# Kernel tuning notes

Hardware: AMD Instinct MI355X
Metric: run time of the kernel (lower is better)

Reference implementation:

```python
import jax, jax.numpy as jnp
import numpy as np

N, G = 10000, 200          # nodes, graphs
EL, EG = 160000, 500000    # local / global edges
S, V = 256, 64             # scalar / vector hidden dims
NA, NB = 16, 5             # atom types, bond types


def _lin(k, i, o):
    return (jax.random.normal(k, (i, o), jnp.float32) / np.sqrt(i))


def scatter_mean(vals, idx, num_segments):
    # vals: [N, ...]; idx: [N] int
    sums = jax.ops.segment_sum(vals, idx, num_segments=num_segments)
    cnt = jax.ops.segment_sum(jnp.ones((vals.shape[0],), vals.dtype), idx,
                              num_segments=num_segments)
    cnt = jnp.maximum(cnt, 1.0).reshape((-1,) + (1,) * (vals.ndim - 1))
    return sums / cnt


def calc_edge_attrs(edge_index, pos):
    src, tgt = edge_index[0], edge_index[1]
    r = pos[tgt] - pos[src]                      # [E,3]
    a = (pos[tgt] * pos[src]).sum(-1)            # [E]
    d = jnp.sqrt(jnp.clip((r ** 2).sum(-1), 1e-6))
    r_norm = r / d[:, None]
    return d, a, r_norm


def setup_inputs() -> dict:
    key = jax.random.key(0)
    ks = jax.random.split(key, 24)
    inp = {}
    inp["x"] = jax.random.normal(ks[0], (N, NA), jnp.float32)
    inp["t"] = jax.random.uniform(ks[1], (G, 1), jnp.float32)
    inp["pos"] = jax.random.normal(ks[2], (N, 3), jnp.float32)
    eil = jax.random.randint(ks[3], (2, EL), 0, N)
    eig = jax.random.randint(ks[4], (2, EG), 0, N)
    # avoid self-edges so edge distances are strictly positive (safe sqrt grads)
    eig = eig.at[1].set(jnp.where(eig[1] == eig[0], (eig[1] + 1) % N, eig[1]))
    eil = eil.at[1].set(jnp.where(eil[1] == eil[0], (eil[1] + 1) % N, eil[1]))
    inp["edge_index_local"] = eil
    inp["edge_index_global"] = eig
    inp["edge_attr_global"] = jax.random.normal(ks[5], (EG, NB), jnp.float32)
    inp["batch"] = jnp.sort(jax.random.randint(ks[6], (N,), 0, G))
    # learned parameters
    inp["W_time"], inp["b_time"] = _lin(ks[7], 1, S), jnp.zeros((S,), jnp.float32)
    inp["W_atom"], inp["b_atom"] = _lin(ks[8], NA, S), jnp.zeros((S,), jnp.float32)
    inp["W_at"], inp["b_at"] = _lin(ks[9], S, S), jnp.zeros((S,), jnp.float32)
    inp["W_shared"], inp["b_shared"] = _lin(ks[10], S, S), jnp.zeros((S,), jnp.float32)
    inp["W_b0"], inp["b_b0"] = _lin(ks[11], S + 1, S), jnp.zeros((S,), jnp.float32)
    inp["W_b1"], inp["b_b1"] = _lin(ks[12], S, 2 * NB), jnp.zeros((2 * NB,), jnp.float32)
    inp["W_coord"] = _lin(ks[13], V, 2)           # no bias
    inp["W_atoms"], inp["b_atoms"] = _lin(ks[14], S, 2 * NA), jnp.zeros((2 * NA,), jnp.float32)
    return inp


def reference(x, t, pos, edge_attr_global, W_time, b_time, W_atom, b_atom,
              W_at, b_at, W_shared, b_shared, W_b0, b_b0, W_b1, b_b1,
              W_coord, W_atoms, b_atoms,
              edge_index_local, edge_index_global, batch):
    # --- trunk: center positions, embed atoms + time ---
    pos = pos - scatter_mean(pos, batch, G)[batch]
    temb = t @ W_time + b_time                    # [G,S]
    tnode = temb[batch]                           # [N,S]
    s = x @ W_atom + b_atom
    s = (s + tnode) @ W_at + b_at                 # [N,S]
    # --- edge attrs (gather-compute pattern feeding the GNN) ---
    d_l, a_l, rn_l = calc_edge_attrs(edge_index_local, pos)
    d_g, a_g, rn_g = calc_edge_attrs(edge_index_global, pos)
    # GNN stand-in (identity on s, v, p): v initialized to zeros as in original
    v = jnp.zeros((N, 3, V), s.dtype)
    # --- prediction head ---
    s = jax.nn.silu(s @ W_shared + b_shared)
    j, i = edge_index_global[0], edge_index_global[1]
    d = jnp.sqrt(((pos[i] - pos[j]) ** 2).sum(-1, keepdims=True))  # [EG,1]
    edge = jnp.concatenate([s[i] + s[j], d], axis=-1)              # [EG,S+1]
    bonds = jax.nn.silu(edge @ W_b0 + b_b0) @ W_b1 + b_b1          # [EG,2*NB]
    bonds_pred, bonds_eps = bonds[:, :NB], bonds[:, NB:]
    coords = jnp.einsum('nkv,vo->nko', v, W_coord)                 # [N,3,2]
    coords = coords - scatter_mean(coords, batch, G)[batch]
    coords_eps0, coords_eps1 = coords[..., 0], coords[..., 1]      # [N,3]
    atoms = s @ W_atoms + b_atoms                                  # [N,2*NA]
    atoms_eps, atoms_pred = atoms[:, :NA], atoms[:, NA:]
    pos_c = pos - scatter_mean(pos, batch, G)[batch]
    coords_pred = pos_c + coords_eps1
    return (coords_pred, coords_eps0, atoms_pred, atoms_eps,
            bonds_pred, bonds_eps, d_l, rn_l, a_g, rn_g)
```

## Files before the change

### kernel.cpp

```cpp
#include <hip/hip_runtime.h>
#include <hip/hip_bf16.h>

typedef __hip_bfloat16 bf16;
typedef short bf16x8 __attribute__((ext_vector_type(8)));
typedef float f32x4 __attribute__((ext_vector_type(4)));
typedef _Float16 f16x2 __attribute__((ext_vector_type(2)));
typedef _Float16 f16x8 __attribute__((ext_vector_type(8)));

#define N_NODES  10000
#define G_GRAPHS 200
#define EL_EDGES 160000
#define EG_EDGES 500000
#define S_DIM    256
#define APAD     264

#define BONDS2        7813
#define LOCAL_BLOCKS  625

#define WS_FLAG   0
#define WS_POSC   1024
#define WS_WDH    31232
#define WS_W1F    31488
#define WS_BB0R   33536
#define WS_BB1    34304
#define WS_WATOM  34560
#define WS_WTIME  38656
#define WS_BTIME  38912
#define WS_BATOM  39168
#define WS_BAT    39424
#define WS_BSH    39680
#define WS_BATOMS 39936
#define WS_T      40000
#define WS_X      40448
#define WT_AT     200448
#define WT_SH     233216
#define WT_B0     265984
#define WT_ATOMS  298752
#define WS_H      303968
#define WS_END_FLOATS 1583968

#define O_CPRED 0
#define O_CEPS  30000
#define O_APRED 60000
#define O_AEPS  220000
#define O_BPRED 380000
#define O_BEPS  2880000
#define O_DL    5380000
#define O_RNL   5540000
#define O_AG    6020000
#define O_RNG   6520000

__device__ __forceinline__ float b2f(bf16 v) { return __bfloat162float(v); }
__device__ __forceinline__ bf16  f2b(float v) { return __float2bfloat16(v); }
__device__ __forceinline__ unsigned short bbits(float v) {
    bf16 b = f2b(v);
    return *reinterpret_cast<unsigned short*>(&b);
}
__device__ __forceinline__ unsigned short h16bits(float v) {
    _Float16 h = (_Float16)v;
    return *reinterpret_cast<unsigned short*>(&h);
}
__device__ __forceinline__ float ldin(const void* p, int idx, int isf32) {
    return isf32 ? ((const float*)p)[idx] : b2f(((const bf16*)p)[idx]);
}
__device__ __forceinline__ void stout(void* out, int f32o, size_t idx, float v) {
    if (f32o) ((float*)out)[idx] = v;
    else      ((bf16*)out)[idx]  = f2b(v);
}
__device__ __forceinline__ float silu(float p) {
    return p * __builtin_amdgcn_rcpf(1.0f + __expf(-p));
}
__device__ __forceinline__ _Float16 h_exp2(_Float16 x) {
    _Float16 r;
    asm("v_exp_f16 %0, %1" : "=v"(r) : "v"(x));
    return r;
}
__device__ __forceinline__ _Float16 h_rcp(_Float16 x) {
    _Float16 r;
    asm("v_rcp_f16 %0, %1" : "=v"(r) : "v"(x));
    return r;
}
__device__ __forceinline__ _Float16 h_silu(_Float16 p) {
    const _Float16 nlog2e = (_Float16)(-1.44269504f);
    _Float16 ex = h_exp2(p * nlog2e);
    return p * h_rcp((_Float16)1.0f + ex);
}
__device__ __forceinline__ int dtype_f32(const void* tt) {
    const unsigned short* q = (const unsigned short*)tt;
    int c = 0;
#pragma unroll
    for (int z = 0; z < 32; ++z) c += (q[z] >= 0x4000) ? 1 : 0;
    return c > 0;
}

__global__ void k_prep(const void* __restrict__ x, const void* __restrict__ tt,
                       const void* __restrict__ W_time, const void* __restrict__ b_time,
                       const void* __restrict__ W_atom, const void* __restrict__ b_atom,
                       const void* __restrict__ W_at, const void* __restrict__ b_at,
                       const void* __restrict__ W_shared, const void* __restrict__ b_shared,
                       const void* __restrict__ W_b0, const void* __restrict__ b_b0,
                       const void* __restrict__ W_b1, const void* __restrict__ b_b1,
                       const void* __restrict__ W_atoms, const void* __restrict__ b_atoms,
                       float* __restrict__ ws) {
    const int t = blockIdx.x * blockDim.x + threadIdx.x;
    const int f = dtype_f32(tt);
    if (t == 0) ws[WS_FLAG] = f ? 1.0f : 0.0f;
    if (t < 65536) {
        const int k = t >> 8, n = t & 255;
        ((unsigned short*)(ws + WT_AT))[n * 256 + k] = bbits(ldin(W_at, t, f));
        ((unsigned short*)(ws + WT_SH))[n * 256 + k] = bbits(ldin(W_shared, t, f));
        ((unsigned short*)(ws + WT_B0))[n * 256 + k] = bbits(ldin(W_b0, t, f));
    }
    if (t < 160000) ws[WS_X + t] = ldin(x, t, f);
    if (t < 8192) {
        const int k = t >> 5, n = t & 31;
        ((unsigned short*)(ws + WT_ATOMS))[n * 256 + k] = bbits(ldin(W_atoms, t, f));
    }
    if (t < 4096) {
        const int i = t & 7, l16 = (t >> 3) & 15, quad = (t >> 7) & 3, ts = t >> 9;
        const int k = ts * 32 + quad * 8 + i;
        float v = (l16 < 10) ? ldin(W_b1, k * 10 + l16, f) : 0.0f;
        ((unsigned short*)(ws + WS_W1F))[t] = h16bits(v);
    }
    if (t < 4096) ws[WS_WATOM + t] = ldin(W_atom, t, f);
    if (t < 256) {
        ((unsigned short*)(ws + WS_WDH))[t] = h16bits(ldin(W_b0, 65536 + t, f));
        ws[WS_BB0R + t] = ldin(b_b0, t, f);
        ws[WS_WTIME + t] = ldin(W_time, t, f);
        ws[WS_BTIME + t] = ldin(b_time, t, f);
        ws[WS_BATOM + t] = ldin(b_atom, t, f);
        ws[WS_BAT + t]   = ldin(b_at, t, f);
        ws[WS_BSH + t]   = ldin(b_shared, t, f);
    }
    if (t < 200) ws[WS_T + t] = ldin(tt, t, f);
    if (t < 32)  ws[WS_BATOMS + t] = ldin(b_atoms, t, f);
    if (t < 16)  ws[WS_BB1 + t] = (t < 10) ? ldin(b_b1, t, f) : 0.0f;
}

__global__ void k_pos(const void* __restrict__ pos, const int* __restrict__ batch,
                      float* __restrict__ ws, void* __restrict__ out) {
    const int g = blockIdx.x;
    const int f32o = ws[WS_FLAG] != 0.0f;
    __shared__ int s_lo, s_hi;
    __shared__ float wsum[4][3];
    __shared__ float mean[3];
    if (threadIdx.x == 0) {
        int lo = 0, hi = N_NODES;
        while (lo < hi) { int m = (lo + hi) >> 1; if (batch[m] < g) lo = m + 1; else hi = m; }
        s_lo = lo;
        int lo2 = lo; hi = N_NODES;
        while (lo2 < hi) { int m = (lo2 + hi) >> 1; if (batch[m] < g + 1) lo2 = m + 1; else hi = m; }
        s_hi = lo2;
    }
    __syncthreads();
    const int lo = s_lo, hi = s_hi, cnt = hi - lo;
    float sx = 0.f, sy = 0.f, sz = 0.f;
    for (int n = lo + threadIdx.x; n < hi; n += 256) {
        sx += ldin(pos, n * 3 + 0, f32o);
        sy += ldin(pos, n * 3 + 1, f32o);
        sz += ldin(pos, n * 3 + 2, f32o);
    }
#pragma unroll
    for (int off = 32; off > 0; off >>= 1) {
        sx += __shfl_down(sx, off);
        sy += __shfl_down(sy, off);
        sz += __shfl_down(sz, off);
    }
    if ((threadIdx.x & 63) == 0) {
        wsum[threadIdx.x >> 6][0] = sx;
        wsum[threadIdx.x >> 6][1] = sy;
        wsum[threadIdx.x >> 6][2] = sz;
    }
    __syncthreads();
    if (threadIdx.x == 0) {
        float inv = 1.0f / (float)max(cnt, 1);
        mean[0] = (wsum[0][0] + wsum[1][0] + wsum[2][0] + wsum[3][0]) * inv;
        mean[1] = (wsum[0][1] + wsum[1][1] + wsum[2][1] + wsum[3][1]) * inv;
        mean[2] = (wsum[0][2] + wsum[1][2] + wsum[2][2] + wsum[3][2]) * inv;
    }
    __syncthreads();
    for (int n = lo + threadIdx.x; n < hi; n += 256) {
#pragma unroll
        for (int k = 0; k < 3; ++k) {
            float p = ldin(pos, n * 3 + k, f32o) - mean[k];
            ws[WS_POSC + n * 3 + k] = p;
            stout(out, f32o, O_CPRED + n * 3 + k, p);
            stout(out, f32o, O_CEPS + n * 3 + k, 0.0f);
        }
    }
}

__global__ __launch_bounds__(256) void k_node(
    const int* __restrict__ batch, const float* __restrict__ ws,
    unsigned short* __restrict__ h_out, void* __restrict__ out) {
    __shared__ unsigned short actA[16][APAD];
    __shared__ unsigned short actB[16][APAD];
    const int tid = threadIdx.x;
    const int wave = tid >> 6, lane = tid & 63;
    const int quad = lane >> 4, l16 = lane & 15;
    const int row0 = blockIdx.x * 16;

    {
        const int r = tid >> 4;
        const int c0 = (tid & 15) * 16;
        const int g = row0 + r;
        float tb = ws[WS_T + batch[g]];
        float xr[16];
#pragma unroll
        for (int k = 0; k < 16; ++k) xr[k] = ws[WS_X + g * 16 + k];
        for (int cc = 0; cc < 16; cc += 4) {
            const int c = c0 + cc;
            float a0 = ws[WS_BATOM + c + 0] + tb * ws[WS_WTIME + c + 0] + ws[WS_BTIME + c + 0];
            float a1 = ws[WS_BATOM + c + 1] + tb * ws[WS_WTIME + c + 1] + ws[WS_BTIME + c + 1];
            float a2 = ws[WS_BATOM + c + 2] + tb * ws[WS_WTIME + c + 2] + ws[WS_BTIME + c + 2];
            float a3 = ws[WS_BATOM + c + 3] + tb * ws[WS_WTIME + c + 3] + ws[WS_BTIME + c + 3];
#pragma unroll
            for (int k = 0; k < 16; ++k) {
                float4 w4 = *(const float4*)(ws + WS_WATOM + k * S_DIM + c);
                a0 += xr[k] * w4.x; a1 += xr[k] * w4.y;
                a2 += xr[k] * w4.z; a3 += xr[k] * w4.w;
            }
            actA[r][c + 0] = bbits(a0); actA[r][c + 1] = bbits(a1);
            actA[r][c + 2] = bbits(a2); actA[r][c + 3] = bbits(a3);
        }
    }
    __syncthreads();

    const unsigned short* wt_at = (const unsigned short*)(ws + WT_AT);
    const unsigned short* wt_sh = (const unsigned short*)(ws + WT_SH);
    const unsigned short* wt_b0 = (const unsigned short*)(ws + WT_B0);
    const unsigned short* wt_am = (const unsigned short*)(ws + WT_ATOMS);
    const int n0 = wave * 64;

    {
        f32x4 acc[4] = {};
        for (int kk = 0; kk < S_DIM; kk += 32) {
            const int k = kk + quad * 8;
            bf16x8 a = *(const bf16x8*)&actA[l16][k];
#pragma unroll
            for (int nt = 0; nt < 4; ++nt) {
                bf16x8 b = *(const bf16x8*)(wt_at + (size_t)(n0 + nt * 16 + l16) * S_DIM + k);
                acc[nt] = __builtin_amdgcn_mfma_f32_16x16x32_bf16(a, b, acc[nt], 0, 0, 0);
            }
        }
#pragma unroll
        for (int nt = 0; nt < 4; ++nt) {
            const int n = n0 + nt * 16 + l16;
            const float bv = ws[WS_BAT + n];
#pragma unroll
            for (int r = 0; r < 4; ++r)
                actB[quad * 4 + r][n] = bbits(acc[nt][r] + bv);
        }
    }
    __syncthreads();

    {
        f32x4 acc[4] = {};
        for (int kk = 0; kk < S_DIM; kk += 32) {
            const int k = kk + quad * 8;
            bf16x8 a = *(const bf16x8*)&actB[l16][k];
#pragma unroll
            for (int nt = 0; nt < 4; ++nt) {
                bf16x8 b = *(const bf16x8*)(wt_sh + (size_t)(n0 + nt * 16 + l16) * S_DIM + k);
                acc[nt] = __builtin_amdgcn_mfma_f32_16x16x32_bf16(a, b, acc[nt], 0, 0, 0);
            }
        }
        __syncthreads();
#pragma unroll
        for (int nt = 0; nt < 4; ++nt) {
            const int n = n0 + nt * 16 + l16;
            const float bv = ws[WS_BSH + n];
#pragma unroll
            for (int r = 0; r < 4; ++r)
                actA[quad * 4 + r][n] = bbits(silu(acc[nt][r] + bv));
        }
    }
    __syncthreads();

    {
        f32x4 acc[4] = {};
        for (int kk = 0; kk < S_DIM; kk += 32) {
            const int k = kk + quad * 8;
            bf16x8 a = *(const bf16x8*)&actA[l16][k];
#pragma unroll
            for (int nt = 0; nt < 4; ++nt) {
                bf16x8 b = *(const bf16x8*)(wt_b0 + (size_t)(n0 + nt * 16 + l16) * S_DIM + k);
                acc[nt] = __builtin_amdgcn_mfma_f32_16x16x32_bf16(a, b, acc[nt], 0, 0, 0);
            }
        }
        _Float16* hp = (_Float16*)h_out;
#pragma unroll
        for (int nt = 0; nt < 4; ++nt) {
            const int n = n0 + nt * 16 + l16;
            const float bh = 0.5f * ws[WS_BB0R + n];
#pragma unroll
            for (int r = 0; r < 4; ++r) {
                const int g = row0 + quad * 4 + r;
                hp[(size_t)g * 256 + n] = (_Float16)(acc[nt][r] + bh);
            }
        }
    }

    if (wave < 2) {
        f32x4 acc = {};
        const int n = wave * 16 + l16;
        for (int kk = 0; kk < S_DIM; kk += 32) {
            const int k = kk + quad * 8;
            bf16x8 a = *(const bf16x8*)&actA[l16][k];
            bf16x8 b = *(const bf16x8*)(wt_am + (size_t)n * S_DIM + k);
            acc = __builtin_amdgcn_mfma_f32_16x16x32_bf16(a, b, acc, 0, 0, 0);
        }
        const float bv = ws[WS_BATOMS + n];
        const int f32o = ws[WS_FLAG] != 0.0f;
#pragma unroll
        for (int r = 0; r < 4; ++r) {
            const int g = row0 + quad * 4 + r;
            float v = acc[r] + bv;
            if (n < 16) stout(out, f32o, O_AEPS + (size_t)g * 16 + n, v);
            else        stout(out, f32o, O_APRED + (size_t)g * 16 + (n - 16), v);
        }
    }
}

union H8 { f16x8 v; f16x2 p[4]; };

__global__ __launch_bounds__(256, 4) void k_edges(const int* __restrict__ eig,
                                                  const int* __restrict__ eil,
                                                  const float* __restrict__ ws,
                                                  const _Float16* __restrict__ h,
                                                  void* __restrict__ out) {
    const int f32o = ws[WS_FLAG] != 0.0f;

    if (blockIdx.x >= BONDS2) {
        const int e = (blockIdx.x - BONDS2) * 256 + threadIdx.x;
        const float* posc = ws + WS_POSC;
        const int s = eil[e];
        const int t = eil[EL_EDGES + e];
        float rx = posc[t * 3 + 0] - posc[s * 3 + 0];
        float ry = posc[t * 3 + 1] - posc[s * 3 + 1];
        float rz = posc[t * 3 + 2] - posc[s * 3 + 2];
        float dsq = rx * rx + ry * ry + rz * rz;
        float d = sqrtf(fmaxf(dsq, 1e-6f));
        float inv = 1.0f / d;
        stout(out, f32o, O_DL + e, d);
        stout(out, f32o, O_RNL + (size_t)e * 3 + 0, rx * inv);
        stout(out, f32o, O_RNL + (size_t)e * 3 + 1, ry * inv);
        stout(out, f32o, O_RNL + (size_t)e * 3 + 2, rz * inv);
        return;
    }

    const int wave = threadIdx.x >> 6, lane = threadIdx.x & 63;
    const int quad = lane >> 4, l16 = lane & 15;
    const int e0 = blockIdx.x * 64 + wave * 16;
    if (e0 >= EG_EDGES) return;

    const int e = e0 + l16;
    const int j = eig[e];
    const int i = eig[EG_EDGES + e];

    const float* posc = ws + WS_POSC;
    float pix = posc[i * 3 + 0], piy = posc[i * 3 + 1], piz = posc[i * 3 + 2];
    float pjx = posc[j * 3 + 0], pjy = posc[j * 3 + 1], pjz = posc[j * 3 + 2];
    float rx = pix - pjx, ry = piy - pjy, rz = piz - pjz;
    float dsq = rx * rx + ry * ry + rz * rz;
    float dbf = sqrtf(dsq);
    if (quad == 0) {
        float ag = pix * pjx + piy * pjy + piz * pjz;
        float inv = 1.0f / sqrtf(fmaxf(dsq, 1e-6f));
        stout(out, f32o, O_AG + e, ag);
        stout(out, f32o, O_RNG + (size_t)e * 3 + 0, rx * inv);
        stout(out, f32o, O_RNG + (size_t)e * 3 + 1, ry * inv);
        stout(out, f32o, O_RNG + (size_t)e * 3 + 2, rz * inv);
    }

    const _Float16 hd = (_Float16)dbf;
    const f16x2 d2 = {hd, hd};

    const _Float16* hi_row = h + (size_t)i * 256 + quad * 8;
    const _Float16* hj_row = h + (size_t)j * 256 + quad * 8;
    const _Float16* wdh = (const _Float16*)(ws + WS_WDH) + quad * 8;
    const _Float16* w1f = (const _Float16*)(ws + WS_W1F) + (quad * 16 + l16) * 8;

    f32x4 acc = {};
#pragma unroll 2
    for (int t = 0; t < 8; ++t) {
        H8 A, B, W;
        A.v = *(const f16x8*)(hi_row + t * 32);
        B.v = *(const f16x8*)(hj_row + t * 32);
        W.v = *(const f16x8*)(wdh + t * 32);
        f16x8 WB = *(const f16x8*)(w1f + t * 512);
        f16x2 p2[4];
#pragma unroll
        for (int pp = 0; pp < 4; ++pp)
            p2[pp] = (A.p[pp] + B.p[pp]) + d2 * W.p[pp];
        f16x8 U = {h_silu(p2[0][0]), h_silu(p2[0][1]),
                   h_silu(p2[1][0]), h_silu(p2[1][1]),
                   h_silu(p2[2][0]), h_silu(p2[2][1]),
                   h_silu(p2[3][0]), h_silu(p2[3][1])};
        acc = __builtin_amdgcn_mfma_f32_16x16x32_f16(U, WB, acc, 0, 0, 0);
    }

    if (l16 < 10) {
        const float bv = ws[WS_BB1 + l16];
#pragma unroll
        for (int r = 0; r < 4; ++r) {
            const int er = e0 + quad * 4 + r;
            float v = acc[r] + bv;
            if (l16 < 5) stout(out, f32o, O_BPRED + (size_t)er * 5 + l16, v);
            else         stout(out, f32o, O_BEPS + (size_t)er * 5 + (l16 - 5), v);
        }
    }
}

extern "C" void kernel_launch(void* const* d_in, const int* in_sizes, int n_in,
                              void* d_out, int out_size, void* d_ws, size_t ws_size,
                              hipStream_t stream) {
    const void* x        = d_in[0];
    const void* t        = d_in[1];
    const void* pos      = d_in[2];
    const int*  eil      = (const int*)d_in[3];
    const int*  eig      = (const int*)d_in[4];
    const int*  batch    = (const int*)d_in[6];
    const void* W_time   = d_in[7];
    const void* b_time   = d_in[8];
    const void* W_atom   = d_in[9];
    const void* b_atom   = d_in[10];
    const void* W_at     = d_in[11];
    const void* b_at     = d_in[12];
    const void* W_shared = d_in[13];
    const void* b_shared = d_in[14];
    const void* W_b0     = d_in[15];
    const void* b_b0     = d_in[16];
    const void* W_b1     = d_in[17];
    const void* b_b1     = d_in[18];
    const void* W_atoms  = d_in[20];
    const void* b_atoms  = d_in[21];
    (void)in_sizes; (void)n_in; (void)out_size;

    const size_t NEED = (size_t)WS_END_FLOATS * sizeof(float);
    if (ws_size < NEED) return;

    float* ws = (float*)d_ws;
    unsigned short* hbuf = (unsigned short*)(ws + WS_H);

    k_prep<<<640, 256, 0, stream>>>(x, t, W_time, b_time, W_atom, b_atom,
                                    W_at, b_at, W_shared, b_shared, W_b0, b_b0,
                                    W_b1, b_b1, W_atoms, b_atoms, ws);
    k_pos<<<G_GRAPHS, 256, 0, stream>>>(pos, batch, ws, d_out);
    k_node<<<N_NODES / 16, 256, 0, stream>>>(batch, ws, hbuf, d_out);
    k_edges<<<BONDS2 + LOCAL_BLOCKS, 256, 0, stream>>>(
        eig, eil, ws, (const _Float16*)hbuf, d_out);
}
```

Baseline: 252.6 us.

## Store per-node bond projection in FP8 and gather it in edge kernel

The per-node bond-layer projection h is now written as packed FP8 (4 bytes per 4 channels) instead of fp16, with a permuted channel layout (CHAN) so each lane's 8 consecutive bytes map onto the MFMA K-slice. The edge kernel gathers 8 bytes per row instead of 16 and unpacks them to f32. It then does the add, distance term and SiLU in f32 before packing to f16 for the MFMA. This halves gather traffic on the dominant 500k-edge random reads and shrinks the workspace. The cost is FP8 quantization error in the hidden activations and extra conversion and f32 ALU work per edge.

```diff
diff --git a/kernel.cpp b/kernel.cpp
--- a/kernel.cpp
+++ b/kernel.cpp
@@ -4,8 +4,10 @@
 typedef __hip_bfloat16 bf16;
 typedef short bf16x8 __attribute__((ext_vector_type(8)));
 typedef float f32x4 __attribute__((ext_vector_type(4)));
+typedef float f32x2 __attribute__((ext_vector_type(2)));
 typedef _Float16 f16x2 __attribute__((ext_vector_type(2)));
 typedef _Float16 f16x8 __attribute__((ext_vector_type(8)));
+typedef __fp16 fp16x2 __attribute__((ext_vector_type(2)));
 
 #define N_NODES  10000
 #define G_GRAPHS 200
@@ -19,7 +21,7 @@
 
 #define WS_FLAG   0
 #define WS_POSC   1024
-#define WS_WDH    31232
+#define WS_WD     31232
 #define WS_W1F    31488
 #define WS_BB0R   33536
 #define WS_BB1    34304
@@ -37,7 +39,9 @@
 #define WT_B0     265984
 #define WT_ATOMS  298752
 #define WS_H      303968
-#define WS_END_FLOATS 1583968
+#define WS_END_FLOATS 944224
+
+#define CHAN(S)    ((((S) >> 6) << 6) + (((S) & 3) << 4) + (((S) & 63) >> 2))
 
 #define O_CPRED 0
 #define O_CEPS  30000
@@ -70,20 +74,11 @@
 __device__ __forceinline__ float silu(float p) {
     return p * __builtin_amdgcn_rcpf(1.0f + __expf(-p));
 }
-__device__ __forceinline__ _Float16 h_exp2(_Float16 x) {
-    _Float16 r;
-    asm("v_exp_f16 %0, %1" : "=v"(r) : "v"(x));
-    return r;
-}
-__device__ __forceinline__ _Float16 h_rcp(_Float16 x) {
-    _Float16 r;
-    asm("v_rcp_f16 %0, %1" : "=v"(r) : "v"(x));
-    return r;
-}
-__device__ __forceinline__ _Float16 h_silu(_Float16 p) {
-    const _Float16 nlog2e = (_Float16)(-1.44269504f);
-    _Float16 ex = h_exp2(p * nlog2e);
-    return p * h_rcp((_Float16)1.0f + ex);
+__device__ __forceinline__ f32x2 silu2(f32x2 p) {
+    f32x2 u;
+    u[0] = p[0] * __builtin_amdgcn_rcpf(1.0f + __expf(-p[0]));
+    u[1] = p[1] * __builtin_amdgcn_rcpf(1.0f + __expf(-p[1]));
+    return u;
 }
 __device__ __forceinline__ int dtype_f32(const void* tt) {
     const unsigned short* q = (const unsigned short*)tt;
@@ -117,14 +112,14 @@
         ((unsigned short*)(ws + WT_ATOMS))[n * 256 + k] = bbits(ldin(W_atoms, t, f));
     }
     if (t < 4096) {
-        const int i = t & 7, l16 = (t >> 3) & 15, quad = (t >> 7) & 3, ts = t >> 9;
-        const int k = ts * 32 + quad * 8 + i;
-        float v = (l16 < 10) ? ldin(W_b1, k * 10 + l16, f) : 0.0f;
+        const int i = t & 7, lc = (t >> 3) & 15, q = (t >> 7) & 3, ts = t >> 9;
+        const int s = ts * 32 + q * 8 + i;
+        float v = (lc < 10) ? ldin(W_b1, CHAN(s) * 10 + lc, f) : 0.0f;
         ((unsigned short*)(ws + WS_W1F))[t] = h16bits(v);
     }
     if (t < 4096) ws[WS_WATOM + t] = ldin(W_atom, t, f);
     if (t < 256) {
-        ((unsigned short*)(ws + WS_WDH))[t] = h16bits(ldin(W_b0, 65536 + t, f));
+        ws[WS_WD + t]   = ldin(W_b0, 65536 + CHAN(t), f);
         ws[WS_BB0R + t] = ldin(b_b0, t, f);
         ws[WS_WTIME + t] = ldin(W_time, t, f);
         ws[WS_BTIME + t] = ldin(b_time, t, f);
@@ -192,7 +187,7 @@
 
 __global__ __launch_bounds__(256) void k_node(
     const int* __restrict__ batch, const float* __restrict__ ws,
-    unsigned short* __restrict__ h_out, void* __restrict__ out) {
+    unsigned int* __restrict__ h_out, void* __restrict__ out) {
     __shared__ unsigned short actA[16][APAD];
     __shared__ unsigned short actB[16][APAD];
     const int tid = threadIdx.x;
@@ -288,16 +283,16 @@
                 acc[nt] = __builtin_amdgcn_mfma_f32_16x16x32_bf16(a, b, acc[nt], 0, 0, 0);
             }
         }
-        _Float16* hp = (_Float16*)h_out;
-#pragma unroll
-        for (int nt = 0; nt < 4; ++nt) {
-            const int n = n0 + nt * 16 + l16;
-            const float bh = 0.5f * ws[WS_BB0R + n];
-#pragma unroll
-            for (int r = 0; r < 4; ++r) {
-                const int g = row0 + quad * 4 + r;
-                hp[(size_t)g * 256 + n] = (_Float16)(acc[nt][r] + bh);
-            }
+        float bh[4];
+#pragma unroll
+        for (int nt = 0; nt < 4; ++nt) bh[nt] = 0.5f * ws[WS_BB0R + n0 + nt * 16 + l16];
+#pragma unroll
+        for (int r = 0; r < 4; ++r) {
+            const int g = row0 + quad * 4 + r;
+            int w = 0;
+            w = __builtin_amdgcn_cvt_pk_fp8_f32(acc[0][r] + bh[0], acc[1][r] + bh[1], w, false);
+            w = __builtin_amdgcn_cvt_pk_fp8_f32(acc[2][r] + bh[2], acc[3][r] + bh[3], w, true);
+            h_out[(size_t)g * 64 + wave * 16 + l16] = (unsigned int)w;
         }
     }
 
@@ -322,12 +317,12 @@
     }
 }
 
-union H8 { f16x8 v; f16x2 p[4]; };
+union U8 { f16x8 v; fp16x2 p[4]; };
 
 __global__ __launch_bounds__(256, 4) void k_edges(const int* __restrict__ eig,
                                                   const int* __restrict__ eil,
                                                   const float* __restrict__ ws,
-                                                  const _Float16* __restrict__ h,
+                                                  const unsigned char* __restrict__ h,
                                                   void* __restrict__ out) {
     const int f32o = ws[WS_FLAG] != 0.0f;
 
@@ -363,7 +358,7 @@
     float pjx = posc[j * 3 + 0], pjy = posc[j * 3 + 1], pjz = posc[j * 3 + 2];
     float rx = pix - pjx, ry = piy - pjy, rz = piz - pjz;
     float dsq = rx * rx + ry * ry + rz * rz;
-    float dbf = sqrtf(dsq);
+    float dgeo = sqrtf(dsq);
     if (quad == 0) {
         float ag = pix * pjx + piy * pjy + piz * pjz;
         float inv = 1.0f / sqrtf(fmaxf(dsq, 1e-6f));
@@ -373,31 +368,42 @@
         stout(out, f32o, O_RNG + (size_t)e * 3 + 2, rz * inv);
     }
 
-    const _Float16 hd = (_Float16)dbf;
-    const f16x2 d2 = {hd, hd};
-
-    const _Float16* hi_row = h + (size_t)i * 256 + quad * 8;
-    const _Float16* hj_row = h + (size_t)j * 256 + quad * 8;
-    const _Float16* wdh = (const _Float16*)(ws + WS_WDH) + quad * 8;
+    const f32x2 d2 = {dgeo, dgeo};
+    const unsigned char* hi_row = h + (size_t)i * 256;
+    const unsigned char* hj_row = h + (size_t)j * 256;
     const _Float16* w1f = (const _Float16*)(ws + WS_W1F) + (quad * 16 + l16) * 8;
 
     f32x4 acc = {};
 #pragma unroll 2
     for (int t = 0; t < 8; ++t) {
-        H8 A, B, W;
-        A.v = *(const f16x8*)(hi_row + t * 32);
-        B.v = *(const f16x8*)(hj_row + t * 32);
-        W.v = *(const f16x8*)(wdh + t * 32);
-        f16x8 WB = *(const f16x8*)(w1f + t * 512);
-        f16x2 p2[4];
-#pragma unroll
-        for (int pp = 0; pp < 4; ++pp)
-            p2[pp] = (A.p[pp] + B.p[pp]) + d2 * W.p[pp];
-        f16x8 U = {h_silu(p2[0][0]), h_silu(p2[0][1]),
-                   h_silu(p2[1][0]), h_silu(p2[1][1]),
-                   h_silu(p2[2][0]), h_silu(p2[2][1]),
-                   h_silu(p2[3][0]), h_silu(p2[3][1])};
-        acc = __builtin_amdgcn_mfma_f32_16x16x32_f16(U, WB, acc, 0, 0, 0);
+        const int k = quad * 8 + t * 32;
+        uint2 ua = *(const uint2*)(hi_row + k);
+        uint2 ub = *(const uint2*)(hj_row + k);
+        float4 wA = *(const float4*)(ws + WS_WD + k);
+        float4 wB = *(const float4*)(ws + WS_WD + k + 4);
+        f16x8 WF = *(const f16x8*)(w1f + t * 512);
+        f32x2 a01 = __builtin_amdgcn_cvt_pk_f32_fp8((int)ua.x, false);
+        f32x2 a23 = __builtin_amdgcn_cvt_pk_f32_fp8((int)ua.x, true);
+        f32x2 a45 = __builtin_amdgcn_cvt_pk_f32_fp8((int)ua.y, false);
+        f32x2 a67 = __builtin_amdgcn_cvt_pk_f32_fp8((int)ua.y, true);
+        f32x2 b01 = __builtin_amdgcn_cvt_pk_f32_fp8((int)ub.x, false);
+        f32x2 b23 = __builtin_amdgcn_cvt_pk_f32_fp8((int)ub.x, true);
+        f32x2 b45 = __builtin_amdgcn_cvt_pk_f32_fp8((int)ub.y, false);
+        f32x2 b67 = __builtin_amdgcn_cvt_pk_f32_fp8((int)ub.y, true);
+        f32x2 p01 = (a01 + b01) + d2 * (f32x2){wA.x, wA.y};
+        f32x2 p23 = (a23 + b23) + d2 * (f32x2){wA.z, wA.w};
+        f32x2 p45 = (a45 + b45) + d2 * (f32x2){wB.x, wB.y};
+        f32x2 p67 = (a67 + b67) + d2 * (f32x2){wB.z, wB.w};
+        f32x2 u01 = silu2(p01);
+        f32x2 u23 = silu2(p23);
+        f32x2 u45 = silu2(p45);
+        f32x2 u67 = silu2(p67);
+        U8 U;
+        U.p[0] = __builtin_amdgcn_cvt_pkrtz(u01[0], u01[1]);
+        U.p[1] = __builtin_amdgcn_cvt_pkrtz(u23[0], u23[1]);
+        U.p[2] = __builtin_amdgcn_cvt_pkrtz(u45[0], u45[1]);
+        U.p[3] = __builtin_amdgcn_cvt_pkrtz(u67[0], u67[1]);
+        acc = __builtin_amdgcn_mfma_f32_16x16x32_f16(U.v, WF, acc, 0, 0, 0);
     }
 
     if (l16 < 10) {
@@ -441,7 +447,7 @@
     if (ws_size < NEED) return;
 
     float* ws = (float*)d_ws;
-    unsigned short* hbuf = (unsigned short*)(ws + WS_H);
+    unsigned int* hbuf = (unsigned int*)(ws + WS_H);
 
     k_prep<<<640, 256, 0, stream>>>(x, t, W_time, b_time, W_atom, b_atom,
                                     W_at, b_at, W_shared, b_shared, W_b0, b_b0,
@@ -449,5 +455,5 @@
     k_pos<<<G_GRAPHS, 256, 0, stream>>>(pos, batch, ws, d_out);
     k_node<<<N_NODES / 16, 256, 0, stream>>>(batch, ws, hbuf, d_out);
     k_edges<<<BONDS2 + LOCAL_BLOCKS, 256, 0, stream>>>(
-        eig, eil, ws, (const _Float16*)hbuf, d_out);
-}
+        eig, eil, ws, (const unsigned char*)hbuf, d_out);
+}
```

After: 259.6 us. 2.8% more time.
